# Kernel optimization log

Hardware: AMD Instinct MI355X
Metric: run time of the kernel (lower is better)

## Reference

```python
import jax, jax.numpy as jnp
import numpy as np

D_MODEL = 1536
BLOCK = 3
N_BLOCKS = D_MODEL // BLOCK
BATCH = 8192
EPS = 1e-8


def setup_inputs() -> dict:
    key = jax.random.key(0)
    ks = jax.random.split(key, 6)
    s = 1.0 / np.sqrt(D_MODEL)  # torch Linear default-ish scale
    x = jax.random.normal(ks[0], (BATCH, D_MODEL), dtype=jnp.float32)
    h_prev = jax.random.normal(ks[1], (BATCH, D_MODEL), dtype=jnp.float32)
    W_biv = jax.random.normal(ks[2], (D_MODEL, D_MODEL), dtype=jnp.float32) * s
    b_biv = jnp.zeros((D_MODEL,), dtype=jnp.float32)  # init.zeros_
    W_dec = jax.random.normal(ks[3], (1, D_MODEL), dtype=jnp.float32) * s
    b_dec = jnp.full((1,), 1.4, dtype=jnp.float32)  # init.constant_(1.4)
    W_in = jax.random.normal(ks[4], (D_MODEL, D_MODEL), dtype=jnp.float32) * s
    b_in = jax.random.normal(ks[5], (D_MODEL,), dtype=jnp.float32) * s
    return {"x": x, "h_prev": h_prev, "W_biv": W_biv, "b_biv": b_biv,
            "W_dec": W_dec, "b_dec": b_dec, "W_in": W_in, "b_in": b_in}


def _quat_rotate_blocks(h_blocks, bivectors):
    # h_blocks, bivectors: (batch, n_blocks, 3)
    norm_b = jnp.maximum(jnp.linalg.norm(bivectors, axis=-1, keepdims=True), EPS)
    half_angle = norm_b / 2
    w = jnp.cos(half_angle)[..., 0]
    s = (jnp.sin(half_angle) / norm_b)[..., 0]  # sin_ha_over_norm[..., 0]
    # NOTE: faithful to source — qx/qy/qz all use component 0 of sin_ha_over_norm
    qx = s * bivectors[..., 2]
    qy = -s * bivectors[..., 1]
    qz = s * bivectors[..., 0]
    vx, vy, vz = h_blocks[..., 0], h_blocks[..., 1], h_blocks[..., 2]
    tx = 2 * (qy * vz - qz * vy)
    ty = 2 * (qz * vx - qx * vz)
    tz = 2 * (qx * vy - qy * vx)
    rx = vx + w * tx + (qy * tz - qz * ty)
    ry = vy + w * ty + (qz * tx - qx * tz)
    rz = vz + w * tz + (qx * ty - qy * tx)
    return jnp.stack([rx, ry, rz], axis=-1)


def reference(x, h_prev, W_biv, b_biv, W_dec, b_dec, W_in, b_in):
    batch = x.shape[0]
    bivectors = (x @ W_biv.T + b_biv).reshape(batch, N_BLOCKS, 3)
    decay = jax.nn.sigmoid(x @ W_dec.T + b_dec)          # (batch, 1)
    injection = x @ W_in.T + b_in                        # (batch, d_model)
    h_blocks = h_prev.reshape(batch, N_BLOCKS, 3)
    rotated = _quat_rotate_blocks(h_blocks, bivectors)
    return decay * rotated.reshape(batch, D_MODEL) + injection
```

## Files before the change

### kernel.cpp

```cpp
#include <hip/hip_runtime.h>
#include <cstdint>

#define D_MODEL 1536
#define BATCH   8192
#define EPS     1e-8f

#define BM 128
#define BN 96
#define BK 64
#define NTN (D_MODEL / BN)
#define NTM (BATCH / BM)

typedef __attribute__((ext_vector_type(8))) short bf16x8;
typedef __attribute__((ext_vector_type(8))) unsigned short ushort8;
typedef __attribute__((ext_vector_type(4))) float f32x4;

__device__ __forceinline__ unsigned short f2bf(float f) {
  unsigned u = __builtin_bit_cast(unsigned, f);
  u += 0x7fffu + ((u >> 16) & 1u);
  return (unsigned short)(u >> 16);
}

__device__ __forceinline__ ushort8 pack8u(float4 a, float4 b) {
  ushort8 o;
  o[0] = f2bf(a.x); o[1] = f2bf(a.y); o[2] = f2bf(a.z); o[3] = f2bf(a.w);
  o[4] = f2bf(b.x); o[5] = f2bf(b.y); o[6] = f2bf(b.z); o[7] = f2bf(b.w);
  return o;
}

__device__ __forceinline__ void full_drain() {
  asm volatile("s_waitcnt vmcnt(0) lgkmcnt(0)" ::: "memory");
}

__device__ __forceinline__ void load_lds16(const void* g, void* l) {
  __builtin_amdgcn_global_load_lds(
      (const __attribute__((address_space(1))) unsigned int*)g,
      (__attribute__((address_space(3))) unsigned int*)l,
      16, 0, 0);
}

__global__ void prep_xd(const float* __restrict__ x,
                        const float* __restrict__ wdec,
                        const float* __restrict__ bdec,
                        unsigned short* __restrict__ xb,
                        float* __restrict__ decay) {
  int row  = (int)((blockIdx.x * blockDim.x + threadIdx.x) >> 6);
  int lane = threadIdx.x & 63;
  if (row >= BATCH) return;
  const float4* xr = (const float4*)(x + (long)row * D_MODEL);
  const float4* wr = (const float4*)wdec;
  unsigned short* xo = xb + (long)row * D_MODEL;
  float acc = 0.f;
#pragma unroll
  for (int i = 0; i < 6; ++i) {
    float4 a = xr[lane + 64 * i];
    float4 b = wr[lane + 64 * i];
    acc += a.x * b.x + a.y * b.y + a.z * b.z + a.w * b.w;
    ushort4 o;
    o.x = f2bf(a.x); o.y = f2bf(a.y); o.z = f2bf(a.z); o.w = f2bf(a.w);
    *(ushort4*)(xo + (lane + 64 * i) * 4) = o;
  }
  for (int off = 32; off; off >>= 1) acc += __shfl_xor(acc, off);
  if (lane == 0) decay[row] = 1.f / (1.f + expf(-(acc + bdec[0])));
}

__global__ void prep_w(const float* __restrict__ wbiv,
                       const float* __restrict__ win,
                       unsigned short* __restrict__ wb) {
  const long NW4 = (long)D_MODEL * D_MODEL / 4;
  for (long i = (long)blockIdx.x * blockDim.x + threadIdx.x; i < 2 * NW4;
       i += (long)gridDim.x * blockDim.x) {
    const float4* src = (i < NW4) ? (const float4*)wbiv : (const float4*)win;
    long j = (i < NW4) ? i : (i - NW4);
    float4 v = src[j];
    ushort4 o;
    o.x = f2bf(v.x); o.y = f2bf(v.y); o.z = f2bf(v.z); o.w = f2bf(v.w);
    *(ushort4*)(wb + 4 * i) = o;
  }
}

__global__ __launch_bounds__(512, 2)
void fused_main(const unsigned short* __restrict__ xb,
                const unsigned short* __restrict__ wb,
                const float* __restrict__ hprev,
                const float* __restrict__ decay,
                const float* __restrict__ bbiv,
                const float* __restrict__ bin,
                float* __restrict__ out) {
  __shared__ __align__(16) char smem[50688];
  __shared__ float sDecay[BM];
  unsigned short* sA  = (unsigned short*)smem;
  unsigned short* sB1 = (unsigned short*)(smem + 16384);
  unsigned short* sB2 = (unsigned short*)(smem + 28672);
  float* sBv = (float*)smem;

  const int bid = blockIdx.x;
  const int tm = bid / NTN, tn = bid % NTN;
  const int m0 = tm * BM, n0 = tn * BN;
  const int tid  = threadIdx.x;
  const int lane = tid & 63, wid = tid >> 6;
  const int wr = wid >> 1, wc = wid & 1;
  const int lr = lane & 15;
  const int lk = lane >> 4;

  if (tid < BM) sDecay[tid] = decay[m0 + tid];

  f32x4 accB[2][3], accI[2][3];
#pragma unroll
  for (int a = 0; a < 2; ++a)
#pragma unroll
    for (int b = 0; b < 3; ++b) { accB[a][b] = (f32x4)0.f; accI[a][b] = (f32x4)0.f; }

  for (int kt = 0; kt < D_MODEL; kt += BK) {
    full_drain();
    __syncthreads();
#pragma unroll
    for (int i = 0; i < 2; ++i) {
      int f = i * 512 + tid;
      int row = f >> 3, c = f & 7;
      int cs = c ^ (row & 7);
      const unsigned short* g = xb + (long)(m0 + row) * D_MODEL + kt + cs * 8;
      load_lds16(g, smem + ((i * 512 + wid * 64) << 4));
    }
    {
      int f = tid;
      int row = f >> 3, c = f & 7, cs = c ^ (row & 7);
      const unsigned short* g = wb + (long)(n0 + row) * D_MODEL + kt + cs * 8;
      load_lds16(g, smem + 16384 + ((wid * 64) << 4));
    }
    if (tid < 256) {
      int f = 512 + tid;
      int row = f >> 3, c = f & 7, cs = c ^ (row & 7);
      const unsigned short* g = wb + (long)(n0 + row) * D_MODEL + kt + cs * 8;
      load_lds16(g, smem + 16384 + ((512 + wid * 64) << 4));
    }
    {
      int f = tid;
      int row = f >> 3, c = f & 7, cs = c ^ (row & 7);
      const unsigned short* g = wb + (long)(D_MODEL + n0 + row) * D_MODEL + kt + cs * 8;
      load_lds16(g, smem + 28672 + ((wid * 64) << 4));
    }
    if (tid < 256) {
      int f = 512 + tid;
      int row = f >> 3, c = f & 7, cs = c ^ (row & 7);
      const unsigned short* g = wb + (long)(D_MODEL + n0 + row) * D_MODEL + kt + cs * 8;
      load_lds16(g, smem + 28672 + ((512 + wid * 64) << 4));
    }
    full_drain();
    __syncthreads();

#pragma unroll
    for (int ks = 0; ks < 2; ++ks) {
      const int slot = ks * 4 + lk;
      bf16x8 a[2], b1[3], b2[3];
#pragma unroll
      for (int mi = 0; mi < 2; ++mi) {
        int R = wr * 32 + mi * 16 + lr;
        a[mi] = *(const bf16x8*)(sA + R * 64 + (slot ^ (R & 7)) * 8);
      }
#pragma unroll
      for (int ni = 0; ni < 3; ++ni) {
        int R = wc * 48 + ni * 16 + lr;
        b1[ni] = *(const bf16x8*)(sB1 + R * 64 + (slot ^ (R & 7)) * 8);
        b2[ni] = *(const bf16x8*)(sB2 + R * 64 + (slot ^ (R & 7)) * 8);
      }
      full_drain();
      __builtin_amdgcn_sched_barrier(0);
#pragma unroll
      for (int mi = 0; mi < 2; ++mi)
#pragma unroll
        for (int ni = 0; ni < 3; ++ni)
          accB[mi][ni] = __builtin_amdgcn_mfma_f32_16x16x32_bf16(
              a[mi], b1[ni], accB[mi][ni], 0, 0, 0);
      __builtin_amdgcn_sched_barrier(0);
#pragma unroll
      for (int mi = 0; mi < 2; ++mi)
#pragma unroll
        for (int ni = 0; ni < 3; ++ni)
          accI[mi][ni] = __builtin_amdgcn_mfma_f32_16x16x32_bf16(
              a[mi], b2[ni], accI[mi][ni], 0, 0, 0);
      __builtin_amdgcn_sched_barrier(0);
    }
  }

  full_drain();
  __syncthreads();
#pragma unroll
  for (int mi = 0; mi < 2; ++mi)
#pragma unroll
    for (int ni = 0; ni < 3; ++ni) {
      int col = wc * 48 + ni * 16 + lr;
      float bb = bbiv[n0 + col];
#pragma unroll
      for (int r = 0; r < 4; ++r) {
        int row = wr * 32 + mi * 16 + lk * 4 + r;
        sBv[row * 97 + col] = accB[mi][ni][r] + bb;
      }
    }
  full_drain();
  __syncthreads();

#pragma unroll
  for (int mi = 0; mi < 2; ++mi)
#pragma unroll
    for (int ni = 0; ni < 3; ++ni) {
      int col  = wc * 48 + ni * 16 + lr;
      int gcol = n0 + col;
      int c    = (col % 3);
      int lc0  = col - c;
      float binv = bin[gcol];
#pragma unroll
      for (int r = 0; r < 4; ++r) {
        int row  = wr * 32 + mi * 16 + lk * 4 + r;
        int grow = m0 + row;
        float bx = sBv[row * 97 + lc0];
        float by = sBv[row * 97 + lc0 + 1];
        float bz = sBv[row * 97 + lc0 + 2];
        const float* hp = hprev + (long)grow * D_MODEL + (n0 + lc0);
        float vx = hp[0], vy = hp[1], vz = hp[2];
        float nb = sqrtf(bx * bx + by * by + bz * bz);
        nb = fmaxf(nb, EPS);
        float ha = 0.5f * nb;
        float w  = cosf(ha);
        float s  = sinf(ha) / nb;
        float qx = s * bz, qy = -s * by, qz = s * bx;
        float tx = 2.f * (qy * vz - qz * vy);
        float ty = 2.f * (qz * vx - qx * vz);
        float tz = 2.f * (qx * vy - qy * vx);
        float rx = vx + w * tx + (qy * tz - qz * ty);
        float ry = vy + w * ty + (qz * tx - qx * tz);
        float rz = vz + w * tz + (qx * ty - qy * tx);
        float rc = (c == 0) ? rx : ((c == 1) ? ry : rz);
        out[(long)grow * D_MODEL + gcol] =
            sDecay[row] * rc + (accI[mi][ni][r] + binv);
      }
    }
}

__global__ __launch_bounds__(256, 2)
void fused_mfma3(const float* __restrict__ x,
                 const float* __restrict__ wbiv,
                 const float* __restrict__ win,
                 const float* __restrict__ hprev,
                 const float* __restrict__ wdec,
                 const float* __restrict__ bdec,
                 const float* __restrict__ bbiv,
                 const float* __restrict__ bin,
                 float* __restrict__ out) {
  __shared__ __align__(16) char smem[50688];
  __shared__ float sDecay[BM];
  unsigned short* sA  = (unsigned short*)smem;
  unsigned short* sB1 = (unsigned short*)(smem + 16384);
  unsigned short* sB2 = (unsigned short*)(smem + 28672);
  float* sBv = (float*)smem;

  const int bid = blockIdx.x;
  const int tm = bid / NTN, tn = bid % NTN;
  const int m0 = tm * BM, n0 = tn * BN;
  const int tid  = threadIdx.x;
  const int lane = tid & 63, wid = tid >> 6;
  const int wr = wid >> 1, wc = wid & 1;
  const int lr = lane & 15;
  const int lk = lane >> 4;

  {
    const float bd = bdec[0];
    const float4* wd4 = (const float4*)wdec;
    for (int rr = 0; rr < 32; ++rr) {
      int row = wid * 32 + rr;
      const float4* xr = (const float4*)(x + (long)(m0 + row) * D_MODEL);
      float acc = 0.f;
#pragma unroll
      for (int i = 0; i < 6; ++i) {
        float4 a = xr[lane + 64 * i];
        float4 b = wd4[lane + 64 * i];
        acc += a.x * b.x + a.y * b.y + a.z * b.z + a.w * b.w;
      }
      for (int off = 32; off; off >>= 1) acc += __shfl_xor(acc, off);
      if (lane == 0) sDecay[row] = 1.f / (1.f + expf(-(acc + bd)));
    }
  }

  f32x4 accB[4][3], accI[4][3];
#pragma unroll
  for (int a = 0; a < 4; ++a)
#pragma unroll
    for (int b = 0; b < 3; ++b) { accB[a][b] = (f32x4)0.f; accI[a][b] = (f32x4)0.f; }

  for (int kt = 0; kt < D_MODEL; kt += BK) {
    full_drain();
    __syncthreads();
#pragma unroll
    for (int i = 0; i < 4; ++i) {
      int f = i * 256 + tid;
      int row = f >> 3, c = f & 7;
      const float4* p = (const float4*)(x + (long)(m0 + row) * D_MODEL + kt + c * 8);
      *(ushort8*)(sA + row * 64 + c * 8) = pack8u(p[0], p[1]);
    }
#pragma unroll
    for (int i = 0; i < 6; ++i) {
      int mat = (i >= 3);
      int g = (i - 3 * mat) * 256 + tid;
      int row = g >> 3, c = g & 7;
      const float* wsrc = mat ? win : wbiv;
      const float4* p = (const float4*)(wsrc + (long)(n0 + row) * D_MODEL + kt + c * 8);
      *(ushort8*)((mat ? sB2 : sB1) + row * 64 + c * 8) = pack8u(p[0], p[1]);
    }
    full_drain();
    __syncthreads();

#pragma unroll
    for (int ks = 0; ks < 2; ++ks) {
      const int k0 = ks * 32 + lk * 8;
      bf16x8 a[4], b1[3], b2[3];
#pragma unroll
      for (int mi = 0; mi < 4; ++mi)
        a[mi] = *(const bf16x8*)(sA + (wr * 64 + mi * 16 + lr) * 64 + k0);
#pragma unroll
      for (int ni = 0; ni < 3; ++ni) {
        b1[ni] = *(const bf16x8*)(sB1 + (wc * 48 + ni * 16 + lr) * 64 + k0);
        b2[ni] = *(const bf16x8*)(sB2 + (wc * 48 + ni * 16 + lr) * 64 + k0);
      }
      full_drain();
      __builtin_amdgcn_sched_barrier(0);
#pragma unroll
      for (int mi = 0; mi < 4; ++mi)
#pragma unroll
        for (int ni = 0; ni < 3; ++ni)
          accB[mi][ni] = __builtin_amdgcn_mfma_f32_16x16x32_bf16(
              a[mi], b1[ni], accB[mi][ni], 0, 0, 0);
      __builtin_amdgcn_sched_barrier(0);
#pragma unroll
      for (int mi = 0; mi < 4; ++mi)
#pragma unroll
        for (int ni = 0; ni < 3; ++ni)
          accI[mi][ni] = __builtin_amdgcn_mfma_f32_16x16x32_bf16(
              a[mi], b2[ni], accI[mi][ni], 0, 0, 0);
      __builtin_amdgcn_sched_barrier(0);
    }
  }

  full_drain();
  __syncthreads();
#pragma unroll
  for (int mi = 0; mi < 4; ++mi)
#pragma unroll
    for (int ni = 0; ni < 3; ++ni) {
      int col = wc * 48 + ni * 16 + lr;
      float bb = bbiv[n0 + col];
#pragma unroll
      for (int r = 0; r < 4; ++r) {
        int row = wr * 64 + mi * 16 + lk * 4 + r;
        sBv[row * 97 + col] = accB[mi][ni][r] + bb;
      }
    }
  full_drain();
  __syncthreads();

#pragma unroll
  for (int mi = 0; mi < 4; ++mi)
#pragma unroll
    for (int ni = 0; ni < 3; ++ni) {
      int col  = wc * 48 + ni * 16 + lr;
      int gcol = n0 + col;
      int c    = (col % 3);
      int lc0  = col - c;
      float binv = bin[gcol];
#pragma unroll
      for (int r = 0; r < 4; ++r) {
        int row  = wr * 64 + mi * 16 + lk * 4 + r;
        int grow = m0 + row;
        float bx = sBv[row * 97 + lc0];
        float by = sBv[row * 97 + lc0 + 1];
        float bz = sBv[row * 97 + lc0 + 2];
        const float* hp = hprev + (long)grow * D_MODEL + (n0 + lc0);
        float vx = hp[0], vy = hp[1], vz = hp[2];
        float nb = sqrtf(bx * bx + by * by + bz * bz);
        nb = fmaxf(nb, EPS);
        float ha = 0.5f * nb;
        float w  = cosf(ha);
        float s  = sinf(ha) / nb;
        float qx = s * bz, qy = -s * by, qz = s * bx;
        float tx = 2.f * (qy * vz - qz * vy);
        float ty = 2.f * (qz * vx - qx * vz);
        float tz = 2.f * (qx * vy - qy * vx);
        float rx = vx + w * tx + (qy * tz - qz * ty);
        float ry = vy + w * ty + (qz * tx - qx * tz);
        float rz = vz + w * tz + (qx * ty - qy * tx);
        float rc = (c == 0) ? rx : ((c == 1) ? ry : rz);
        out[(long)grow * D_MODEL + gcol] =
            sDecay[row] * rc + (accI[mi][ni][r] + binv);
      }
    }
}

extern "C" void kernel_launch(void* const* d_in, const int* in_sizes, int n_in,
                              void* d_out, int out_size, void* d_ws, size_t ws_size,
                              hipStream_t stream) {
  const float* x     = (const float*)d_in[0];
  const float* hprev = (const float*)d_in[1];
  const float* wbiv  = (const float*)d_in[2];
  const float* bbiv  = (const float*)d_in[3];
  const float* wdec  = (const float*)d_in[4];
  const float* bdec  = (const float*)d_in[5];
  const float* win   = (const float*)d_in[6];
  const float* bin   = (const float*)d_in[7];
  float* out = (float*)d_out;

  const size_t XB_B  = 25165824;
  const size_t WB_B  = 9437184;
  const size_t DC_B  = 32768;

  if (ws_size >= XB_B + WB_B + DC_B) {
    char* ws = (char*)d_ws;
    unsigned short* xb = (unsigned short*)ws;
    unsigned short* wb = (unsigned short*)(ws + XB_B);
    float* decay       = (float*)(ws + XB_B + WB_B);
    prep_xd<<<dim3(2048), dim3(256), 0, stream>>>(x, wdec, bdec, xb, decay);
    prep_w<<<dim3(1024), dim3(256), 0, stream>>>(wbiv, win, wb);
    fused_main<<<dim3(NTM * NTN), dim3(512), 0, stream>>>(
        xb, wb, hprev, decay, bbiv, bin, out);
  } else {
    fused_mfma3<<<dim3(NTM * NTN), dim3(256), 0, stream>>>(
        x, wbiv, win, hprev, wdec, bdec, bbiv, bin, out);
  }
}
```

Before: 126.0 us.

## Double-buffer LDS tiles to overlap global loads with MFMA compute

```diff
diff --git a/kernel.cpp b/kernel.cpp
--- a/kernel.cpp
+++ b/kernel.cpp
@@ -8,8 +8,10 @@
 #define BM 128
 #define BN 96
 #define BK 64
+#define NT (D_MODEL / BK)
 #define NTN (D_MODEL / BN)
 #define NTM (BATCH / BM)
+#define BUF 40960
 
 typedef __attribute__((ext_vector_type(8))) short bf16x8;
 typedef __attribute__((ext_vector_type(8))) unsigned short ushort8;
@@ -30,6 +32,12 @@
 
 __device__ __forceinline__ void full_drain() {
   asm volatile("s_waitcnt vmcnt(0) lgkmcnt(0)" ::: "memory");
+}
+__device__ __forceinline__ void vm_drain() {
+  asm volatile("s_waitcnt vmcnt(0)" ::: "memory");
+}
+__device__ __forceinline__ void lgkm_drain() {
+  asm volatile("s_waitcnt lgkmcnt(0)" ::: "memory");
 }
 
 __device__ __forceinline__ void load_lds16(const void* g, void* l) {
@@ -87,11 +95,7 @@
                 const float* __restrict__ bbiv,
                 const float* __restrict__ bin,
                 float* __restrict__ out) {
-  __shared__ __align__(16) char smem[50688];
-  __shared__ float sDecay[BM];
-  unsigned short* sA  = (unsigned short*)smem;
-  unsigned short* sB1 = (unsigned short*)(smem + 16384);
-  unsigned short* sB2 = (unsigned short*)(smem + 28672);
+  __shared__ __align__(16) char smem[2 * BUF];
   float* sBv = (float*)smem;
 
   const int bid = blockIdx.x;
@@ -103,51 +107,58 @@
   const int lr = lane & 15;
   const int lk = lane >> 4;
 
-  if (tid < BM) sDecay[tid] = decay[m0 + tid];
-
   f32x4 accB[2][3], accI[2][3];
 #pragma unroll
   for (int a = 0; a < 2; ++a)
 #pragma unroll
     for (int b = 0; b < 3; ++b) { accB[a][b] = (f32x4)0.f; accI[a][b] = (f32x4)0.f; }
 
-  for (int kt = 0; kt < D_MODEL; kt += BK) {
-    full_drain();
-    __syncthreads();
+  auto STAGE = [&](int kt, int bb) {
 #pragma unroll
     for (int i = 0; i < 2; ++i) {
       int f = i * 512 + tid;
       int row = f >> 3, c = f & 7;
       int cs = c ^ (row & 7);
       const unsigned short* g = xb + (long)(m0 + row) * D_MODEL + kt + cs * 8;
-      load_lds16(g, smem + ((i * 512 + wid * 64) << 4));
+      load_lds16(g, smem + bb + ((i * 512 + wid * 64) << 4));
     }
     {
       int f = tid;
       int row = f >> 3, c = f & 7, cs = c ^ (row & 7);
       const unsigned short* g = wb + (long)(n0 + row) * D_MODEL + kt + cs * 8;
-      load_lds16(g, smem + 16384 + ((wid * 64) << 4));
+      load_lds16(g, smem + bb + 16384 + ((wid * 64) << 4));
     }
     if (tid < 256) {
       int f = 512 + tid;
       int row = f >> 3, c = f & 7, cs = c ^ (row & 7);
       const unsigned short* g = wb + (long)(n0 + row) * D_MODEL + kt + cs * 8;
-      load_lds16(g, smem + 16384 + ((512 + wid * 64) << 4));
+      load_lds16(g, smem + bb + 16384 + ((512 + wid * 64) << 4));
     }
     {
       int f = tid;
       int row = f >> 3, c = f & 7, cs = c ^ (row & 7);
       const unsigned short* g = wb + (long)(D_MODEL + n0 + row) * D_MODEL + kt + cs * 8;
-      load_lds16(g, smem + 28672 + ((wid * 64) << 4));
+      load_lds16(g, smem + bb + 28672 + ((wid * 64) << 4));
     }
     if (tid < 256) {
       int f = 512 + tid;
       int row = f >> 3, c = f & 7, cs = c ^ (row & 7);
       const unsigned short* g = wb + (long)(D_MODEL + n0 + row) * D_MODEL + kt + cs * 8;
-      load_lds16(g, smem + 28672 + ((512 + wid * 64) << 4));
-    }
-    full_drain();
-    __syncthreads();
+      load_lds16(g, smem + bb + 28672 + ((512 + wid * 64) << 4));
+    }
+  };
+
+  STAGE(0, 0);
+  vm_drain();
+  __syncthreads();
+
+  for (int t = 0; t < NT; ++t) {
+    const int cur = (t & 1) * BUF;
+    if (t + 1 < NT) STAGE((t + 1) * BK, ((t + 1) & 1) * BUF);
+
+    const unsigned short* cA  = (const unsigned short*)(smem + cur);
+    const unsigned short* cB1 = (const unsigned short*)(smem + cur + 16384);
+    const unsigned short* cB2 = (const unsigned short*)(smem + cur + 28672);
 
 #pragma unroll
     for (int ks = 0; ks < 2; ++ks) {
@@ -156,15 +167,15 @@
 #pragma unroll
       for (int mi = 0; mi < 2; ++mi) {
         int R = wr * 32 + mi * 16 + lr;
-        a[mi] = *(const bf16x8*)(sA + R * 64 + (slot ^ (R & 7)) * 8);
+        a[mi] = *(const bf16x8*)(cA + R * 64 + (slot ^ (R & 7)) * 8);
       }
 #pragma unroll
       for (int ni = 0; ni < 3; ++ni) {
         int R = wc * 48 + ni * 16 + lr;
-        b1[ni] = *(const bf16x8*)(sB1 + R * 64 + (slot ^ (R & 7)) * 8);
-        b2[ni] = *(const bf16x8*)(sB2 + R * 64 + (slot ^ (R & 7)) * 8);
-      }
-      full_drain();
+        b1[ni] = *(const bf16x8*)(cB1 + R * 64 + (slot ^ (R & 7)) * 8);
+        b2[ni] = *(const bf16x8*)(cB2 + R * 64 + (slot ^ (R & 7)) * 8);
+      }
+      lgkm_drain();
       __builtin_amdgcn_sched_barrier(0);
 #pragma unroll
       for (int mi = 0; mi < 2; ++mi)
@@ -181,10 +192,11 @@
               a[mi], b2[ni], accI[mi][ni], 0, 0, 0);
       __builtin_amdgcn_sched_barrier(0);
     }
-  }
-
-  full_drain();
-  __syncthreads();
+
+    vm_drain();
+    __syncthreads();
+  }
+
 #pragma unroll
   for (int mi = 0; mi < 2; ++mi)
 #pragma unroll
@@ -232,7 +244,7 @@
         float rz = vz + w * tz + (qx * ty - qy * tx);
         float rc = (c == 0) ? rx : ((c == 1) ? ry : rz);
         out[(long)grow * D_MODEL + gcol] =
-            sDecay[row] * rc + (accI[mi][ni][r] + binv);
+            decay[grow] * rc + (accI[mi][ni][r] + binv);
       }
     }
 }
```

Measured after the change: 125.2 us. No clear change (-0.6%).
